# Optimization experiments

Measured on AMD Instinct MI355X. Metric: run time of the kernel, lower is better.

The kernel has to match this reference:

```python
import jax, jax.numpy as jnp
import numpy as np

B, H, W, C = 16, 32, 32, 512
NUM_HEADS = 8
ATTN_DIM = 512
HEAD_DIM = ATTN_DIM // NUM_HEADS
EPS = 1e-5


def setup_inputs() -> dict:
    key = jax.random.key(0)
    ks = jax.random.split(key, 6)
    s_in = 1.0 / np.sqrt(C)
    s_attn = 1.0 / np.sqrt(ATTN_DIM)
    return {
        "x": jax.random.normal(ks[0], (B, H, W, C), dtype=jnp.float32),
        "gamma": jnp.ones((C,), dtype=jnp.float32),
        "beta": jnp.zeros((C,), dtype=jnp.float32),
        "wq": jax.random.normal(ks[1], (C, ATTN_DIM), dtype=jnp.float32) * s_in,
        "bq": jnp.zeros((ATTN_DIM,), dtype=jnp.float32),
        "wk": jax.random.normal(ks[2], (C, ATTN_DIM), dtype=jnp.float32) * s_in,
        "bk": jnp.zeros((ATTN_DIM,), dtype=jnp.float32),
        "wv": jax.random.normal(ks[3], (C, ATTN_DIM), dtype=jnp.float32) * s_in,
        "bv": jnp.zeros((ATTN_DIM,), dtype=jnp.float32),
        "wo": jax.random.normal(ks[4], (ATTN_DIM, C), dtype=jnp.float32) * s_attn,
        "bo": jnp.zeros((C,), dtype=jnp.float32),
    }


def reference(x, gamma, beta, wq, bq, wk, bk, wv, bv, wo, bo):
    b, h, w, c = x.shape
    t = h * w  # number of spatial tokens
    # GroupNorm with 1 group: normalize over (H, W, C) per sample
    mean = jnp.mean(x, axis=(1, 2, 3), keepdims=True)
    var = jnp.var(x, axis=(1, 2, 3), keepdims=True)
    xn = (x - mean) * jax.lax.rsqrt(var + EPS) * gamma + beta
    xn = xn.reshape(b, t, c)
    # 1x1-conv q/k/v == dense over channel dim; split into heads
    q = (xn @ wq + bq).reshape(b, t, NUM_HEADS, HEAD_DIM)
    k = (xn @ wk + bk).reshape(b, t, NUM_HEADS, HEAD_DIM)
    v = (xn @ wv + bv).reshape(b, t, NUM_HEADS, HEAD_DIM)
    scale = 1.0 / jnp.sqrt(jnp.asarray(HEAD_DIM, dtype=x.dtype))
    scores = jnp.einsum('bqhd,bkhd->bhqk', q, k) * scale
    probs = jax.nn.softmax(scores, axis=-1)
    attn = jnp.einsum('bhqk,bkhd->bqhd', probs, v).reshape(b, t, ATTN_DIM)
    out = attn @ wo + bo
    # Multiplex([None, branch]): residual add, then Reshape([-1, model_dim])
    return x.reshape(b, t, c) + out
```

## Files before the change

kernel.cpp:

```cpp
#include <hip/hip_runtime.h>
#include <hip/hip_bf16.h>

typedef __attribute__((ext_vector_type(8))) short short8;
typedef __attribute__((ext_vector_type(4))) short short4v;
typedef __attribute__((ext_vector_type(4))) float f32x4;

#define B_ 16
#define T_ 1024
#define C_ 512
#define NH 8
#define HD 64

__device__ __forceinline__ short f2bf(float f) {
  union { float f; unsigned u; } v;
  v.f = f;
  unsigned r = v.u + 0x7fffu + ((v.u >> 16) & 1u);
  return (short)(r >> 16);
}

__device__ __forceinline__ short2 pack_bf2(float a, float b) {
  __hip_bfloat162 t = __float22bfloat162_rn(make_float2(a, b));
  short2 r;
  __builtin_memcpy(&r, &t, 4);
  return r;
}

__device__ __forceinline__ float fexp2(float x) {
  float r;
  asm("v_exp_f32 %0, %1" : "=v"(r) : "v"(x));
  return r;
}

__device__ __forceinline__ void gload_lds16(const short* g, short* l) {
  __builtin_amdgcn_global_load_lds(
      (const __attribute__((address_space(1))) void*)g,
      (__attribute__((address_space(3))) void*)l, 16, 0, 0);
}

__global__ __launch_bounds__(256) void stats1_trans_kernel(
    const float* __restrict__ x, float2* __restrict__ partials,
    const float* __restrict__ wq, const float* __restrict__ wk,
    const float* __restrict__ wv, const float* __restrict__ wo,
    short* __restrict__ wqkvT, short* __restrict__ woT) {
  int blk = blockIdx.x;
  int tid = threadIdx.x;
  if (blk < 1024) {
    int chunk = blk & 63;
    int b = blk >> 6;
    const float4* xb = (const float4*)(x + (size_t)b * 524288 + (size_t)chunk * 8192);
    float s = 0.f, s2 = 0.f;
#pragma unroll
    for (int i = 0; i < 8; i++) {
      float4 v = xb[tid + i * 256];
      s  += v.x + v.y + v.z + v.w;
      s2 += v.x * v.x + v.y * v.y + v.z * v.z + v.w * v.w;
    }
    __shared__ float ls[256], ls2[256];
    ls[tid] = s; ls2[tid] = s2;
    __syncthreads();
    for (int o = 128; o > 0; o >>= 1) {
      if (tid < o) { ls[tid] += ls[tid + o]; ls2[tid] += ls2[tid + o]; }
      __syncthreads();
    }
    if (tid == 0) partials[b * 64 + chunk] = make_float2(ls[0], ls2[0]);
  } else {
    int o = (blk - 1024) * 256 + tid;
    int sel = o >> 18;
    int oo = o & 262143;
    int k = oo >> 9, n = oo & 511;
    const float* w = (sel == 0) ? wq : (sel == 1) ? wk : (sel == 2) ? wv : wo;
    float val = w[oo];
    if (sel < 3) wqkvT[((size_t)(sel * 512 + n)) * 512 + k] = f2bf(val);
    else         woT[(size_t)n * 512 + k] = f2bf(val);
  }
}

__global__ __launch_bounds__(256) void norm_kernel(const float* __restrict__ x,
                                                   const float* __restrict__ gamma,
                                                   const float* __restrict__ beta,
                                                   const float2* __restrict__ partials,
                                                   short* __restrict__ xn) {
  __shared__ float sm[2];
  int tid = threadIdx.x;
  int b = blockIdx.x >> 7;
  if (tid < 64) {
    float2 p = partials[b * 64 + tid];
    float s = p.x, s2 = p.y;
#pragma unroll
    for (int off = 1; off < 64; off <<= 1) {
      s  += __shfl_xor(s,  off, 64);
      s2 += __shfl_xor(s2, off, 64);
    }
    if (tid == 0) {
      float mean = s * (1.f / 524288.f);
      float var  = s2 * (1.f / 524288.f) - mean * mean;
      sm[0] = mean;
      sm[1] = rsqrtf(var + 1e-5f);
    }
  }
  __syncthreads();
  float mean = sm[0], rstd = sm[1];
#pragma unroll
  for (int it = 0; it < 4; it++) {
    size_t i4 = (size_t)blockIdx.x * 1024 + it * 256 + tid;
    float4 v = ((const float4*)x)[i4];
    int c = (int)((i4 * 4) & 511);
    short4v o;
    o[0] = f2bf((v.x - mean) * rstd * gamma[c + 0] + beta[c + 0]);
    o[1] = f2bf((v.y - mean) * rstd * gamma[c + 1] + beta[c + 1]);
    o[2] = f2bf((v.z - mean) * rstd * gamma[c + 2] + beta[c + 2]);
    o[3] = f2bf((v.w - mean) * rstd * gamma[c + 3] + beta[c + 3]);
    ((short4v*)xn)[i4] = o;
  }
}

__global__ __launch_bounds__(256) void gemm_qkv(const short* __restrict__ A,
                                                const short* __restrict__ Bt,
                                                const float* __restrict__ bq,
                                                const float* __restrict__ bk,
                                                const float* __restrict__ bv,
                                                short* __restrict__ C,
                                                short* __restrict__ vT) {
  __shared__ __align__(16) short As[2][128 * 32];
  __shared__ __align__(16) short Bs[2][128 * 32];
  int tid = threadIdx.x;
  int w = tid >> 6, lane = tid & 63;
  int quad = lane >> 4, l16 = lane & 15;
  int mw = (w >> 1) * 64, nw = (w & 1) * 64;
  int lin = blockIdx.y * 12 + blockIdx.x;
  int my = (lin & 7) + ((lin / 96) << 3);
  int mx = (lin >> 3) % 12;
  int seg = (mx * 128) >> 9;
  const float* bias = (seg == 0) ? bq : (seg == 1) ? bk : bv;
  float smul = (seg == 0) ? 0.18033688011112042f : 1.0f;
  const short* Atile = A + (size_t)(my * 128) * 512;
  const short* Btile = Bt + (size_t)(mx * 128) * 512;
  int srow = (w << 4) + (lane >> 2);
  int scol = (lane & 3) * 8;
  f32x4 acc[4][4] = {};
  for (int k0 = 0; k0 < 512; k0 += 64) {
    __syncthreads();
    gload_lds16(&Atile[(size_t)srow * 512 + k0 + scol],             &As[0][w * 512]);
    gload_lds16(&Atile[(size_t)(srow + 64) * 512 + k0 + scol],      &As[0][2048 + w * 512]);
    gload_lds16(&Atile[(size_t)srow * 512 + k0 + 32 + scol],        &As[1][w * 512]);
    gload_lds16(&Atile[(size_t)(srow + 64) * 512 + k0 + 32 + scol], &As[1][2048 + w * 512]);
    gload_lds16(&Btile[(size_t)srow * 512 + k0 + scol],             &Bs[0][w * 512]);
    gload_lds16(&Btile[(size_t)(srow + 64) * 512 + k0 + scol],      &Bs[0][2048 + w * 512]);
    gload_lds16(&Btile[(size_t)srow * 512 + k0 + 32 + scol],        &Bs[1][w * 512]);
    gload_lds16(&Btile[(size_t)(srow + 64) * 512 + k0 + 32 + scol], &Bs[1][2048 + w * 512]);
    __syncthreads();
    short8 af[2][4], bf[2][4];
#pragma unroll
    for (int s = 0; s < 2; s++)
#pragma unroll
      for (int i = 0; i < 4; i++) {
        af[s][i] = *(const short8*)(&As[s][(mw + i * 16 + l16) * 32 + quad * 8]);
        bf[s][i] = *(const short8*)(&Bs[s][(nw + i * 16 + l16) * 32 + quad * 8]);
      }
#pragma unroll
    for (int mi = 0; mi < 4; mi++)
#pragma unroll
      for (int ni = 0; ni < 4; ni++) {
        acc[mi][ni] = __builtin_amdgcn_mfma_f32_16x16x32_bf16(af[0][mi], bf[0][ni], acc[mi][ni], 0, 0, 0);
        acc[mi][ni] = __builtin_amdgcn_mfma_f32_16x16x32_bf16(af[1][mi], bf[1][ni], acc[mi][ni], 0, 0, 0);
      }
  }
  int m0 = my * 128 + mw;
  int n0 = mx * 128 + nw;
  if (seg < 2) {
#pragma unroll
    for (int mi = 0; mi < 4; mi++)
#pragma unroll
      for (int ni = 0; ni < 4; ni++) {
        int col = n0 + ni * 16 + l16;
        float bval = bias[col & 511];
#pragma unroll
        for (int r = 0; r < 4; r++) {
          int row = m0 + mi * 16 + quad * 4 + r;
          C[(size_t)row * 1024 + col] = f2bf((acc[mi][ni][r] + bval) * smul);
        }
      }
  } else {
    int b = my >> 3;
    int chunk = my & 7;
    int half = mw >> 6;
#pragma unroll
    for (int mi = 0; mi < 4; mi++)
#pragma unroll
      for (int ni = 0; ni < 4; ni++) {
        int c = (n0 - 1024) + ni * 16 + l16;
        int h = c >> 6, d = c & 63;
        float bval = bias[c];
        short4v pk;
#pragma unroll
        for (int r = 0; r < 4; r++) pk[r] = f2bf(acc[mi][ni][r] + bval);
        short* dst = vT + ((size_t)((b * 8 + h) * 64 + d)) * 1024
                        + chunk * 128 + mi * 32 + quad * 8 + half * 4;
        *(short4v*)dst = pk;
      }
  }
}

__global__ __launch_bounds__(256) void gemm_out(const short* __restrict__ A,
                                                const short* __restrict__ Bt,
                                                const float* __restrict__ bias,
                                                const float* __restrict__ xres,
                                                float* __restrict__ out) {
  __shared__ __align__(16) short As[2][128 * 32];
  __shared__ __align__(16) short Bs[2][128 * 32];
  int tid = threadIdx.x;
  int w = tid >> 6, lane = tid & 63;
  int quad = lane >> 4, l16 = lane & 15;
  int mw = (w >> 1) * 64, nw = (w & 1) * 64;
  int lin = blockIdx.y * 4 + blockIdx.x;
  int my = (lin & 7) + ((lin / 32) << 3);
  int mx = (lin >> 3) & 3;
  const short* Atile = A + (size_t)(my * 128) * 512;
  const short* Btile = Bt + (size_t)(mx * 128) * 512;
  int srow = (w << 4) + (lane >> 2);
  int scol = (lane & 3) * 8;
  f32x4 acc[4][4] = {};
  for (int k0 = 0; k0 < 512; k0 += 64) {
    __syncthreads();
    gload_lds16(&Atile[(size_t)srow * 512 + k0 + scol],             &As[0][w * 512]);
    gload_lds16(&Atile[(size_t)(srow + 64) * 512 + k0 + scol],      &As[0][2048 + w * 512]);
    gload_lds16(&Atile[(size_t)srow * 512 + k0 + 32 + scol],        &As[1][w * 512]);
    gload_lds16(&Atile[(size_t)(srow + 64) * 512 + k0 + 32 + scol], &As[1][2048 + w * 512]);
    gload_lds16(&Btile[(size_t)srow * 512 + k0 + scol],             &Bs[0][w * 512]);
    gload_lds16(&Btile[(size_t)(srow + 64) * 512 + k0 + scol],      &Bs[0][2048 + w * 512]);
    gload_lds16(&Btile[(size_t)srow * 512 + k0 + 32 + scol],        &Bs[1][w * 512]);
    gload_lds16(&Btile[(size_t)(srow + 64) * 512 + k0 + 32 + scol], &Bs[1][2048 + w * 512]);
    __syncthreads();
    short8 af[2][4], bf[2][4];
#pragma unroll
    for (int s = 0; s < 2; s++)
#pragma unroll
      for (int i = 0; i < 4; i++) {
        af[s][i] = *(const short8*)(&As[s][(mw + i * 16 + l16) * 32 + quad * 8]);
        bf[s][i] = *(const short8*)(&Bs[s][(nw + i * 16 + l16) * 32 + quad * 8]);
      }
#pragma unroll
    for (int mi = 0; mi < 4; mi++)
#pragma unroll
      for (int ni = 0; ni < 4; ni++) {
        acc[mi][ni] = __builtin_amdgcn_mfma_f32_16x16x32_bf16(af[0][mi], bf[0][ni], acc[mi][ni], 0, 0, 0);
        acc[mi][ni] = __builtin_amdgcn_mfma_f32_16x16x32_bf16(af[1][mi], bf[1][ni], acc[mi][ni], 0, 0, 0);
      }
  }
  int m0 = my * 128 + mw;
  int n0 = mx * 128 + nw;
#pragma unroll
  for (int mi = 0; mi < 4; mi++)
#pragma unroll
    for (int ni = 0; ni < 4; ni++) {
      int col = n0 + ni * 16 + l16;
      float bval = bias[col];
#pragma unroll
      for (int r = 0; r < 4; r++) {
        int row = m0 + mi * 16 + quad * 4 + r;
        out[(size_t)row * 512 + col] = acc[mi][ni][r] + bval + xres[(size_t)row * 512 + col];
      }
    }
}

__global__ __launch_bounds__(256) void attn_kernel(const short* __restrict__ Q,
                                                   const short* __restrict__ Kmat,
                                                   const short* __restrict__ vTg,
                                                   short* __restrict__ O) {
  int tid = threadIdx.x;
  int w = tid >> 6, lane = tid & 63;
  int quad = lane >> 4, l16 = lane & 15;
  int lin = blockIdx.y * 128 + blockIdx.x;
  int bh = (lin & 7) * 16 + (lin >> 7);
  int qt = (lin >> 3) & 15;
  int b = bh >> 3, h = bh & 7;
  size_t base  = ((size_t)b * T_) * 1024 + (size_t)h * 64;
  size_t vbase = ((size_t)bh * 64) * 1024;
  size_t obase = ((size_t)b * T_) * 512 + (size_t)h * 64;
  int qrow0 = qt * 64;

  __shared__ __align__(16) char smem[32768];
  short* KTb[2];
  KTb[0] = (short*)smem;
  KTb[1] = (short*)(smem + 16384);
  float* Lbuf = (float*)smem;

  short8 qf0[4], qf1[4];
#pragma unroll
  for (int g = 0; g < 4; g++) {
    const short* qp = Q + base + (size_t)(qrow0 + g * 16 + l16) * 1024 + quad * 8;
    qf0[g] = *(const short8*)qp;
    qf1[g] = *(const short8*)(qp + 32);
  }

  const short* ksrc[4];
#pragma unroll
  for (int n = 0; n < 4; n++) {
    int bk = w * 256 + n * 64 + lane;
    int key = bk >> 3, jc = bk & 7;
    int dcol = jc ^ (key & 7);
    ksrc[n] = Kmat + base + (size_t)key * 1024 + dcol * 8;
  }

  const short* vp0 = vTg + vbase + (size_t)l16 * 1024 + (w * 4 + quad) * 8;

  int l7 = l16 & 7;
  int kA0 = ((w * 16 + l16) * 8 + (quad ^ l7)) * 8;
  int kA1 = ((w * 16 + l16) * 8 + ((quad + 4) ^ l7)) * 8;
  int kB0 = kA0 + 4096;
  int kB1 = kA1 + 4096;

  f32x4 oacc[4][4] = {};
  float lsum[4] = {0.f, 0.f, 0.f, 0.f};

#pragma unroll
  for (int n = 0; n < 4; n++)
    gload_lds16(ksrc[n], KTb[0] + (w * 256 + n * 64) * 8);

#pragma unroll
  for (int t = 0; t < 8; t++) {
    short* KTc = KTb[t & 1];
    short* KTn = KTb[(t + 1) & 1];
    __syncthreads();
    short8 vfr[4];
#pragma unroll
    for (int f = 0; f < 4; f++)
      vfr[f] = *(const short8*)(vp0 + (size_t)f * 16384 + t * 128);
    if (t < 7) {
#pragma unroll
      for (int n = 0; n < 4; n++)
        gload_lds16(ksrc[n] + (size_t)(t + 1) * 131072, KTn + (w * 256 + n * 64) * 8);
    }
    short8 ka0 = *(const short8*)(KTc + kA0);
    short8 ka1 = *(const short8*)(KTc + kA1);
    short8 kb0 = *(const short8*)(KTc + kB0);
    short8 kb1 = *(const short8*)(KTc + kB1);

#pragma unroll
    for (int g = 0; g < 4; g++) {
      f32x4 za = {}, zb = {};
      __builtin_amdgcn_s_setprio(1);
      za = __builtin_amdgcn_mfma_f32_16x16x32_bf16(ka0, qf0[g], za, 0, 0, 0);
      za = __builtin_amdgcn_mfma_f32_16x16x32_bf16(ka1, qf1[g], za, 0, 0, 0);
      zb = __builtin_amdgcn_mfma_f32_16x16x32_bf16(kb0, qf0[g], zb, 0, 0, 0);
      zb = __builtin_amdgcn_mfma_f32_16x16x32_bf16(kb1, qf1[g], zb, 0, 0, 0);
      __builtin_amdgcn_s_setprio(0);
      float pa0 = fexp2(za[0]), pa1 = fexp2(za[1]);
      float pa2 = fexp2(za[2]), pa3 = fexp2(za[3]);
      float pb0 = fexp2(zb[0]), pb1 = fexp2(zb[1]);
      float pb2 = fexp2(zb[2]), pb3 = fexp2(zb[3]);
      lsum[g] += (pa0 + pa1) + (pa2 + pa3) + ((pb0 + pb1) + (pb2 + pb3));
      short2 a01 = pack_bf2(pa0, pa1), a23 = pack_bf2(pa2, pa3);
      short2 b01 = pack_bf2(pb0, pb1), b23 = pack_bf2(pb2, pb3);
      short8 pf;
      pf[0] = a01.x; pf[1] = a01.y; pf[2] = a23.x; pf[3] = a23.y;
      pf[4] = b01.x; pf[5] = b01.y; pf[6] = b23.x; pf[7] = b23.y;
      __builtin_amdgcn_s_setprio(1);
#pragma unroll
      for (int f = 0; f < 4; f++)
        oacc[f][g] = __builtin_amdgcn_mfma_f32_16x16x32_bf16(vfr[f], pf, oacc[f][g], 0, 0, 0);
      __builtin_amdgcn_s_setprio(0);
    }
  }

#pragma unroll
  for (int g = 0; g < 4; g++) {
    lsum[g] += __shfl_xor(lsum[g], 16, 64);
    lsum[g] += __shfl_xor(lsum[g], 32, 64);
  }
  __syncthreads();
  if (quad == 0) {
#pragma unroll
    for (int g = 0; g < 4; g++)
      Lbuf[(g * 16 + l16) * 68 + 64 + w] = lsum[g];
  }
  for (int ww = 0; ww < 4; ww++) {
    __syncthreads();
    if (w == ww) {
#pragma unroll
      for (int g = 0; g < 4; g++)
#pragma unroll
        for (int f = 0; f < 4; f++) {
          float* p = &Lbuf[(g * 16 + l16) * 68 + f * 16 + quad * 4];
          if (ww == 0) *(f32x4*)p = oacc[f][g];
          else         *(f32x4*)p = *(f32x4*)p + oacc[f][g];
        }
    }
  }
  __syncthreads();

  int q = tid >> 2, seg = tid & 3;
  float4 dnv = *(const float4*)(&Lbuf[q * 68 + 64]);
  float dn = (dnv.x + dnv.y) + (dnv.z + dnv.w);
  float rinv = __frcp_rn(dn);
  const float* row = &Lbuf[q * 68 + seg * 16];
  short8 o0, o1;
#pragma unroll
  for (int i = 0; i < 8; i++) o0[i] = f2bf(row[i] * rinv);
#pragma unroll
  for (int i = 0; i < 8; i++) o1[i] = f2bf(row[8 + i] * rinv);
  short* op = O + obase + (size_t)(qrow0 + q) * 512 + seg * 16;
  *(short8*)op = o0;
  *(short8*)(op + 8) = o1;
}

extern "C" void kernel_launch(void* const* d_in, const int* in_sizes, int n_in,
                              void* d_out, int out_size, void* d_ws, size_t ws_size,
                              hipStream_t stream) {
  const float* x     = (const float*)d_in[0];
  const float* gamma = (const float*)d_in[1];
  const float* beta  = (const float*)d_in[2];
  const float* wq    = (const float*)d_in[3];
  const float* bq    = (const float*)d_in[4];
  const float* wk    = (const float*)d_in[5];
  const float* bk    = (const float*)d_in[6];
  const float* wv    = (const float*)d_in[7];
  const float* bv    = (const float*)d_in[8];
  const float* wo    = (const float*)d_in[9];
  const float* bo    = (const float*)d_in[10];
  float* out = (float*)d_out;

  char* ws = (char*)d_ws;
  const size_t XN_ELEMS = (size_t)B_ * T_ * C_;
  size_t off = 0;
  off += 256;
  float2* partials = (float2*)(ws + off); off += 16 * 64 * sizeof(float2);
  short* xn    = (short*)(ws + off); off += XN_ELEMS * 2;
  short* wqkvT = (short*)(ws + off); off += (size_t)1536 * 512 * 2;
  short* woT   = (short*)(ws + off); off += (size_t)512 * 512 * 2;
  short* qkv   = (short*)(ws + off); off += (size_t)B_ * T_ * 1024 * 2;
  short* vTb   = (short*)(ws + off); off += XN_ELEMS * 2;
  short* ao    = (short*)(ws + off); off += XN_ELEMS * 2;

  stats1_trans_kernel<<<5120, 256, 0, stream>>>(x, partials, wq, wk, wv, wo, wqkvT, woT);
  norm_kernel<<<2048, 256, 0, stream>>>(x, gamma, beta, partials, xn);

  gemm_qkv<<<dim3(12, 128), 256, 0, stream>>>(xn, wqkvT, bq, bk, bv, qkv, vTb);

  attn_kernel<<<dim3(128, 16), 256, 0, stream>>>(qkv, qkv + 512, vTb, ao);

  gemm_out<<<dim3(4, 128), 256, 0, stream>>>(ao, woT, bo, x, out);
}
```

Measured before the change: 225.7 us.

## Fuse stats and norm kernels via cooperative grid sync keeping x in registers

Merges the GroupNorm statistics kernel and the normalization kernel into one cooperative kernel of 1024 blocks. Each block keeps its slice of x in registers across a grid-wide barrier, so x is read from global memory only once, and the weight transpose work is folded into the same blocks. This removes one kernel launch and a full second read of x (32 MB). In exchange the kernel needs a cooperative launch with all 1024 blocks resident at once, which the launch-bounds occupancy hint of 4 blocks per CU targets, and it pays for a grid-sync barrier.

New measurement: 361.9 us. 1.6x slower.

```diff
diff --git a/kernel.cpp b/kernel.cpp
--- a/kernel.cpp
+++ b/kernel.cpp
@@ -1,5 +1,6 @@
 #include <hip/hip_runtime.h>
 #include <hip/hip_bf16.h>
+#include <hip/hip_cooperative_groups.h>
 
 typedef __attribute__((ext_vector_type(8))) short short8;
 typedef __attribute__((ext_vector_type(4))) short short4v;
@@ -37,80 +38,78 @@
       (__attribute__((address_space(3))) void*)l, 16, 0, 0);
 }
 
-__global__ __launch_bounds__(256) void stats1_trans_kernel(
-    const float* __restrict__ x, float2* __restrict__ partials,
+__global__ __launch_bounds__(256, 4) void statsnorm_kernel(
+    const float* __restrict__ x, const float* __restrict__ gamma,
+    const float* __restrict__ beta,
     const float* __restrict__ wq, const float* __restrict__ wk,
     const float* __restrict__ wv, const float* __restrict__ wo,
-    short* __restrict__ wqkvT, short* __restrict__ woT) {
+    short* __restrict__ wqkvT, short* __restrict__ woT,
+    float2* __restrict__ partials, short* __restrict__ xn) {
+  int tid = threadIdx.x;
   int blk = blockIdx.x;
-  int tid = threadIdx.x;
-  if (blk < 1024) {
-    int chunk = blk & 63;
-    int b = blk >> 6;
-    const float4* xb = (const float4*)(x + (size_t)b * 524288 + (size_t)chunk * 8192);
-    float s = 0.f, s2 = 0.f;
-#pragma unroll
-    for (int i = 0; i < 8; i++) {
-      float4 v = xb[tid + i * 256];
-      s  += v.x + v.y + v.z + v.w;
-      s2 += v.x * v.x + v.y * v.y + v.z * v.z + v.w * v.w;
-    }
-    __shared__ float ls[256], ls2[256];
-    ls[tid] = s; ls2[tid] = s2;
-    __syncthreads();
-    for (int o = 128; o > 0; o >>= 1) {
-      if (tid < o) { ls[tid] += ls[tid + o]; ls2[tid] += ls2[tid + o]; }
-      __syncthreads();
-    }
-    if (tid == 0) partials[b * 64 + chunk] = make_float2(ls[0], ls2[0]);
-  } else {
-    int o = (blk - 1024) * 256 + tid;
+  int b = blk >> 6;
+  size_t base4 = (size_t)blk * 2048 + tid;
+  const float4* x4 = (const float4*)x;
+  float4 v[8];
+  float s = 0.f, s2 = 0.f;
+#pragma unroll
+  for (int i = 0; i < 8; i++) {
+    v[i] = x4[base4 + i * 256];
+    s  += v[i].x + v[i].y + v[i].z + v[i].w;
+    s2 += v[i].x * v[i].x + v[i].y * v[i].y + v[i].z * v[i].z + v[i].w * v[i].w;
+  }
+  __shared__ float ls[256], ls2[256];
+  __shared__ float sm[2];
+  ls[tid] = s; ls2[tid] = s2;
+  __syncthreads();
+  for (int o = 128; o > 0; o >>= 1) {
+    if (tid < o) { ls[tid] += ls[tid + o]; ls2[tid] += ls2[tid + o]; }
+    __syncthreads();
+  }
+  if (tid == 0) partials[blk] = make_float2(ls[0], ls2[0]);
+#pragma unroll
+  for (int k2 = 0; k2 < 4; k2++) {
+    int o = blk * 1024 + k2 * 256 + tid;
     int sel = o >> 18;
     int oo = o & 262143;
-    int k = oo >> 9, n = oo & 511;
+    int kk = oo >> 9, n = oo & 511;
     const float* w = (sel == 0) ? wq : (sel == 1) ? wk : (sel == 2) ? wv : wo;
     float val = w[oo];
-    if (sel < 3) wqkvT[((size_t)(sel * 512 + n)) * 512 + k] = f2bf(val);
-    else         woT[(size_t)n * 512 + k] = f2bf(val);
-  }
-}
-
-__global__ __launch_bounds__(256) void norm_kernel(const float* __restrict__ x,
-                                                   const float* __restrict__ gamma,
-                                                   const float* __restrict__ beta,
-                                                   const float2* __restrict__ partials,
-                                                   short* __restrict__ xn) {
-  __shared__ float sm[2];
-  int tid = threadIdx.x;
-  int b = blockIdx.x >> 7;
+    if (sel < 3) wqkvT[((size_t)(sel * 512 + n)) * 512 + kk] = f2bf(val);
+    else         woT[(size_t)n * 512 + kk] = f2bf(val);
+  }
+
+  cooperative_groups::this_grid().sync();
+
   if (tid < 64) {
     float2 p = partials[b * 64 + tid];
-    float s = p.x, s2 = p.y;
+    float ss = p.x, ss2 = p.y;
 #pragma unroll
     for (int off = 1; off < 64; off <<= 1) {
-      s  += __shfl_xor(s,  off, 64);
-      s2 += __shfl_xor(s2, off, 64);
+      ss  += __shfl_xor(ss,  off, 64);
+      ss2 += __shfl_xor(ss2, off, 64);
     }
     if (tid == 0) {
-      float mean = s * (1.f / 524288.f);
-      float var  = s2 * (1.f / 524288.f) - mean * mean;
+      float mean = ss * (1.f / 524288.f);
+      float var  = ss2 * (1.f / 524288.f) - mean * mean;
       sm[0] = mean;
       sm[1] = rsqrtf(var + 1e-5f);
     }
   }
   __syncthreads();
   float mean = sm[0], rstd = sm[1];
-#pragma unroll
-  for (int it = 0; it < 4; it++) {
-    size_t i4 = (size_t)blockIdx.x * 1024 + it * 256 + tid;
-    float4 v = ((const float4*)x)[i4];
-    int c = (int)((i4 * 4) & 511);
-    short4v o;
-    o[0] = f2bf((v.x - mean) * rstd * gamma[c + 0] + beta[c + 0]);
-    o[1] = f2bf((v.y - mean) * rstd * gamma[c + 1] + beta[c + 1]);
-    o[2] = f2bf((v.z - mean) * rstd * gamma[c + 2] + beta[c + 2]);
-    o[3] = f2bf((v.w - mean) * rstd * gamma[c + 3] + beta[c + 3]);
-    ((short4v*)xn)[i4] = o;
+  int c = (int)((tid * 4) & 511);
+  float g0 = gamma[c + 0], g1 = gamma[c + 1], g2 = gamma[c + 2], g3 = gamma[c + 3];
+  float b0 = beta[c + 0],  b1 = beta[c + 1],  b2 = beta[c + 2],  b3 = beta[c + 3];
+#pragma unroll
+  for (int i = 0; i < 8; i++) {
+    size_t i4 = base4 + i * 256;
+    short4v o4;
+    o4[0] = f2bf((v[i].x - mean) * rstd * g0 + b0);
+    o4[1] = f2bf((v[i].y - mean) * rstd * g1 + b1);
+    o4[2] = f2bf((v[i].z - mean) * rstd * g2 + b2);
+    o4[3] = f2bf((v[i].w - mean) * rstd * g3 + b3);
+    ((short4v*)xn)[i4] = o4;
   }
 }
 
@@ -424,7 +423,7 @@
   const size_t XN_ELEMS = (size_t)B_ * T_ * C_;
   size_t off = 0;
   off += 256;
-  float2* partials = (float2*)(ws + off); off += 16 * 64 * sizeof(float2);
+  float2* partials = (float2*)(ws + off); off += 1024 * sizeof(float2);
   short* xn    = (short*)(ws + off); off += XN_ELEMS * 2;
   short* wqkvT = (short*)(ws + off); off += (size_t)1536 * 512 * 2;
   short* woT   = (short*)(ws + off); off += (size_t)512 * 512 * 2;
@@ -432,8 +431,11 @@
   short* vTb   = (short*)(ws + off); off += XN_ELEMS * 2;
   short* ao    = (short*)(ws + off); off += XN_ELEMS * 2;
 
-  stats1_trans_kernel<<<5120, 256, 0, stream>>>(x, partials, wq, wk, wv, wo, wqkvT, woT);
-  norm_kernel<<<2048, 256, 0, stream>>>(x, gamma, beta, partials, xn);
+  void* args[] = {(void*)&x, (void*)&gamma, (void*)&beta,
+                  (void*)&wq, (void*)&wk, (void*)&wv, (void*)&wo,
+                  (void*)&wqkvT, (void*)&woT, (void*)&partials, (void*)&xn};
+  hipLaunchCooperativeKernel((void*)statsnorm_kernel, dim3(1024), dim3(256),
+                             args, 0, stream);
 
   gemm_qkv<<<dim3(12, 128), 256, 0, stream>>>(xn, wqkvT, bq, bk, bv, qkv, vTb);
 
```
